# Kernel tuning notes

Measured on AMD Instinct MI355X. Metric: run time of the kernel, lower is better.

Reference implementation:

```python
import jax, jax.numpy as jnp
import numpy as np

B = 64        # num_groups
G = 32        # group_size
D = 2000      # output dim (counts per bin/gene)
M = 16        # m_samples
E = 16        # noise_dim
DIN = 256
LAM = 1.0
TRUST = 0.25
SMOOTH = 1e-8
IPF_ITERS = 60
EPS = 1e-12


def _arch(x, noise, W, b):
    # simple linear architecture: concat(x, noise) @ W + b
    return jnp.concatenate([x, noise], axis=-1) @ W + b


def _loss(x, target, W, b, noise_loss):
    # replicate each row m times (unsqueeze(1).expand(...).reshape == repeat)
    x_rep = jnp.repeat(x, M, axis=0)                      # [n*M, DIN]
    pred = _arch(x_rep, noise_loss, W, b)                 # [n*M, D] (no act_fn in loss path)
    pred = pred.reshape(B, G, M, D).sum(axis=1)           # [B, M, D]
    term_conf = jnp.linalg.norm(pred - target[:, None, :], axis=2).mean(axis=1)  # [B]
    sq = jnp.sum(pred * pred, axis=2)                     # [B, M]
    inn = jnp.einsum('bmd,bnd->bmn', pred, pred)          # [B, M, M]
    sqd = jnp.clip(sq[:, :, None] + sq[:, None, :] - 2.0 * inn, 1e-6)
    d = jnp.sqrt(sqd)
    mask = 1.0 - jnp.eye(M, dtype=d.dtype)
    mean_pd = jnp.sum(d * mask, axis=(1, 2)) / (M * (M - 1))
    return jnp.mean(term_conf - (LAM / 2.0) * mean_pd)


def _ipf(x_pred, C):
    # KL/I-projection with row anchoring (keep_rows=True, trust_clip=0.25)
    y = jnp.clip(x_pred, 0.0)
    C = jnp.clip(C.astype(y.dtype), 0.0)
    R = y.sum(axis=2)                                     # [B, G] anchor row totals
    col_zero = (y.sum(axis=1) <= 0) & (C > 0)
    y = y + SMOOTH * col_zero[:, None, :].astype(y.dtype)
    row_zero = (y.sum(axis=2) <= 0) & (R > 0)
    y = y + SMOOTH * row_zero[:, :, None].astype(y.dtype)

    def body(_, y):
        col = jnp.clip(y.sum(axis=1), EPS)
        y = y * jnp.clip(C / col, 1.0 - TRUST, 1.0 + TRUST)[:, None, :]
        row = jnp.clip(y.sum(axis=2), EPS)
        y = y * jnp.clip(R / row, 1.0 - TRUST, 1.0 + TRUST)[:, :, None]
        return y

    y = jax.lax.fori_loop(0, IPF_ITERS, body, y)
    col = jnp.clip(y.sum(axis=1), EPS)
    return y * (C / col)[:, None, :]


def _rank(v, descending):
    # rank along last axis via double argsort (0 = first picked)
    order = jnp.argsort(-v if descending else v, axis=-1)
    return jnp.argsort(order, axis=-1)


def _round_to_targets(x, target_bd):
    # exact integerization across G per (B, D); jit-safe full-G rank replaces dynamic-k topk+scatter
    x = jnp.clip(x, 0.0)
    xf = jnp.floor(x)
    y = xf.astype(jnp.int32)                              # [B, G, D]
    frac = x - xf
    need = target_bd - y.sum(axis=1)                      # [B, D]
    pos = jnp.clip(need, 0)
    q = pos // G
    y = y + q[:, None, :]
    r = pos - q * G
    rank = _rank(jnp.transpose(frac, (0, 2, 1)), descending=True)   # [B, D, G]
    add = (rank < r[:, :, None]).astype(jnp.int32)
    y = y + jnp.transpose(add, (0, 2, 1))
    # negative residuals: remove from smallest frac among y > 0
    need = target_bd - y.sum(axis=1)
    neg = jnp.clip(-need, 0)
    neg = jnp.minimum(neg, y.sum(axis=1))
    q = neg // G
    y_before = y
    y = jnp.clip(y - q[:, None, :], 0)
    removed = (y_before - y).sum(axis=1)
    r = neg - removed
    frac_m = jnp.where(y > 0, frac, jnp.inf)
    rank = _rank(jnp.transpose(frac_m, (0, 2, 1)), descending=False)
    rem = (rank < r[:, :, None]).astype(jnp.int32)
    y = jnp.clip(y - jnp.transpose(rem, (0, 2, 1)), 0)
    return y


def setup_inputs() -> dict:
    key = jax.random.key(0)
    ks = jax.random.split(key, 6)
    x = jax.random.normal(ks[0], (B * G, DIN), dtype=jnp.float32)
    target = jax.random.uniform(ks[1], (B, D), dtype=jnp.float32) * 100.0
    target_sum = jax.random.randint(ks[2], (B, D), 0, 200, dtype=jnp.int32)
    W = jax.random.normal(ks[3], (DIN + E, D), dtype=jnp.float32) * 0.02
    b = jnp.zeros((D,), dtype=jnp.float32)
    noise_loss = jax.random.normal(ks[4], (B * G * M, E), dtype=jnp.float32)
    noise_sample = jax.random.normal(ks[5], (B * G, E), dtype=jnp.float32)
    return {"x": x, "target": target, "target_sum": target_sum, "W": W, "b": b,
            "noise_loss": noise_loss, "noise_sample": noise_sample}


def reference(x, target, target_sum, W, b, noise_loss, noise_sample):
    loss = _loss(x, target, W, b, noise_loss)
    # conditional_sample pipeline (no-grad in original): softplus act (min_value==0)
    x_pred = jax.nn.softplus(_arch(x, noise_sample, W, b)).reshape(B, G, D)
    y_float = _ipf(x_pred, target_sum.astype(jnp.float32))
    y_int = _round_to_targets(y_float, target_sum.astype(jnp.int32))
    return loss, y_int.reshape(B * G, D)
```

## Files before the change

kernel.cpp:

```cpp
#include <hip/hip_runtime.h>
#include <math.h>

#define NB   64
#define NG   32
#define ND   2000
#define NM   16
#define NE   16
#define NDIN 256
#define NK   272

__device__ __forceinline__ float clampf(float v, float lo, float hi) {
    return fminf(fmaxf(v, lo), hi);
}

__device__ __forceinline__ float softplusf(float v) {
    return (v > 20.f) ? v : log1pf(expf(v));
}

__device__ __forceinline__ float readlane_f(float v, int lane) {
    return __int_as_float(__builtin_amdgcn_readlane(__float_as_int(v), lane));
}

__device__ __forceinline__ float wave_sum32(float v[NG], int lane) {
    {   const bool hi = (lane & 32) != 0;
        #pragma unroll
        for (int k = 0; k < 16; ++k) {
            float s = hi ? v[k] : v[k + 16];
            float r = __shfl_xor(s, 32);
            v[k] = (hi ? v[k + 16] : v[k]) + r;
        }
    }
    {   const bool hi = (lane & 16) != 0;
        #pragma unroll
        for (int k = 0; k < 8; ++k) {
            float s = hi ? v[k] : v[k + 8];
            float r = __shfl_xor(s, 16);
            v[k] = (hi ? v[k + 8] : v[k]) + r;
        }
    }
    {   const bool hi = (lane & 8) != 0;
        #pragma unroll
        for (int k = 0; k < 4; ++k) {
            float s = hi ? v[k] : v[k + 4];
            float r = __shfl_xor(s, 8);
            v[k] = (hi ? v[k + 4] : v[k]) + r;
        }
    }
    {   const bool hi = (lane & 4) != 0;
        #pragma unroll
        for (int k = 0; k < 2; ++k) {
            float s = hi ? v[k] : v[k + 2];
            float r = __shfl_xor(s, 4);
            v[k] = (hi ? v[k + 2] : v[k]) + r;
        }
    }
    {   const bool hi = (lane & 2) != 0;
        float s = hi ? v[0] : v[1];
        float r = __shfl_xor(s, 2);
        v[0] = (hi ? v[1] : v[0]) + r;
    }
    v[0] += __shfl_xor(v[0], 1);
    return v[0];
}

extern "C" __global__ __launch_bounds__(512)
void k_front(const float* __restrict__ x, const float* __restrict__ nl,
             const float* __restrict__ tgt, const float* __restrict__ W,
             const float* __restrict__ bias, const float* __restrict__ nsamp,
             float* __restrict__ xp, float* __restrict__ res2) {
    __shared__ __align__(16) float xr[NG * NK];
    __shared__ __align__(16) float ls[4800];
    const int q  = blockIdx.x;
    const int cx = q & 7, b = q >> 3;
    const int t  = threadIdx.x;

    for (int idx = t; idx < NG * NK; idx += 512) {
        const int g = idx / NK, c = idx - g * NK;
        const int row = b * NG + g;
        xr[idx] = (c < NDIN) ? x[(size_t)row * NDIN + c]
                             : nsamp[(size_t)row * NE + (c - NDIN)];
    }
    __syncthreads();

    if (t < 500) {
        const int d  = cx * 250 + (t >> 1);
        const int r0 = (t & 1) << 4;
        float acc[16];
        #pragma unroll
        for (int r = 0; r < 16; ++r) acc[r] = 0.f;
        for (int k = 0; k < NK; k += 4) {
            const float w0 = W[(size_t)(k + 0) * ND + d];
            const float w1 = W[(size_t)(k + 1) * ND + d];
            const float w2 = W[(size_t)(k + 2) * ND + d];
            const float w3 = W[(size_t)(k + 3) * ND + d];
            #pragma unroll
            for (int r = 0; r < 16; ++r) {
                const float4 xv = *(const float4*)&xr[(r0 + r) * NK + k];
                acc[r] += xv.x * w0 + xv.y * w1 + xv.z * w2 + xv.w * w3;
            }
        }
        const float bv = bias[d];
        #pragma unroll
        for (int r = 0; r < 16; ++r)
            xp[(size_t)(b * NG + r0 + r) * ND + d] = softplusf(acc[r] + bv);
    }

    if (t < 256) {
        float s = 0.f;
        for (int g = 0; g < NG; ++g) s += xr[g * NK + t];
        ls[t] = s;
        const float* nb = nl + (size_t)b * NG * (NM * NE);
        float s2 = 0.f;
        for (int g = 0; g < NG; ++g) s2 += nb[g * (NM * NE) + t];
        ls[256 + t] = s2;
    }

    int tm = 0, tn = 0;
    if (t >= 16 && t < 152) {
        int p = t - 16;
        for (int m = 0; m < NM; ++m) {
            int c = NM - m;
            if (p < c) { tm = m; tn = m + p; break; }
            p -= c;
        }
    }
    __syncthreads();

    float* xsl = ls;
    float* nsl = ls + 256;
    float* tgl = ls + 512;
    float* pt  = ls + 764;

    const int d = cx * 250 + t;
    if (t < 250) {
        tgl[t] = tgt[b * ND + d];
        float xw = 0.f;
        #pragma unroll 8
        for (int k = 0; k < NDIN; ++k) xw += xsl[k] * W[(size_t)k * ND + d];
        float we[NE];
        #pragma unroll
        for (int e = 0; e < NE; ++e) we[e] = W[(size_t)(NDIN + e) * ND + d];
        const float base0 = xw + (float)NG * bias[d];
        #pragma unroll
        for (int m = 0; m < NM; ++m) {
            float pm = base0;
            #pragma unroll
            for (int e = 0; e < NE; ++e) pm += nsl[m * NE + e] * we[e];
            pt[m * 252 + t] = pm;
        }
    }
    if (t < 32) {
        pt[(t >> 1) * 252 + 250 + (t & 1)] = 0.f;
        if (t < 2) tgl[250 + t] = 0.f;
    }
    __syncthreads();

    float acc = 0.f;
    if (t < 16) {
        const float4* pa  = (const float4*)&pt[t * 252];
        const float4* tga = (const float4*)&tgl[0];
        for (int i = 0; i < 63; ++i) {
            float4 pv = pa[i], tv = tga[i];
            float e0 = pv.x - tv.x, e1 = pv.y - tv.y, e2 = pv.z - tv.z, e3 = pv.w - tv.w;
            acc += e0 * e0 + e1 * e1 + e2 * e2 + e3 * e3;
        }
    } else if (t < 152) {
        const float4* pa = (const float4*)&pt[tm * 252];
        const float4* pb = (const float4*)&pt[tn * 252];
        for (int i = 0; i < 63; ++i) {
            float4 u = pa[i], v = pb[i];
            acc += u.x * v.x + u.y * v.y + u.z * v.z + u.w * v.w;
        }
    }
    if (t < 152) res2[((size_t)b * 8 + cx) * 152 + t] = acc;
}

__device__ __forceinline__ void ipf_path(
        const float* __restrict__ xp, const int* __restrict__ tsum,
        float* __restrict__ out, float* smem, int b, int t) {
    const int lane = t & 63, w = t >> 6;
    const int d0 = t * 4;
    const bool valid = (d0 < ND);
    const int g_own = (lane >> 1) & 31;

    float* wred = smem;

    float y0r[4][NG];
    #pragma unroll
    for (int g = 0; g < NG; ++g) {
        float4 v = make_float4(0.f, 0.f, 0.f, 0.f);
        if (valid) v = *(const float4*)(xp + (size_t)(b * NG + g) * ND + d0);
        y0r[0][g] = fmaxf(v.x, 0.f);
        y0r[1][g] = fmaxf(v.y, 0.f);
        y0r[2][g] = fmaxf(v.z, 0.f);
        y0r[3][g] = fmaxf(v.w, 0.f);
    }
    float Cc[4] = {0.f, 0.f, 0.f, 0.f};
    if (valid) {
        const int4 ci = *(const int4*)(tsum + (size_t)b * ND + d0);
        Cc[0] = (float)ci.x; Cc[1] = (float)ci.y; Cc[2] = (float)ci.z; Cc[3] = (float)ci.w;
    }
    float Ac[4] = {1.f, 1.f, 1.f, 1.f};
    float Bown = 1.f;
    float Rown;

    {
        float v[NG];
        #pragma unroll
        for (int g = 0; g < NG; ++g)
            v[g] = y0r[0][g] + y0r[1][g] + y0r[2][g] + y0r[3][g];
        const float tot = wave_sum32(v, lane);
        if ((lane & 1) == 0) wred[w * NG + g_own] = tot;
        __syncthreads();
        float s = 0.f;
        #pragma unroll
        for (int w2 = 0; w2 < 8; ++w2) s += wred[w2 * NG + g_own];
        Rown = s;
    }

    for (int q = 1; q <= 60; ++q) {
        float s0 = 0.f, s1 = 0.f, s2 = 0.f, s3 = 0.f;
        #pragma unroll
        for (int g = 0; g < NG; ++g) {
            const float bg = readlane_f(Bown, 2 * g);
            s0 += y0r[0][g] * bg; s1 += y0r[1][g] * bg;
            s2 += y0r[2][g] * bg; s3 += y0r[3][g] * bg;
        }
        Ac[0] *= clampf(Cc[0] / fmaxf(Ac[0] * s0, 1e-12f), 0.75f, 1.25f);
        Ac[1] *= clampf(Cc[1] / fmaxf(Ac[1] * s1, 1e-12f), 0.75f, 1.25f);
        Ac[2] *= clampf(Cc[2] / fmaxf(Ac[2] * s2, 1e-12f), 0.75f, 1.25f);
        Ac[3] *= clampf(Cc[3] / fmaxf(Ac[3] * s3, 1e-12f), 0.75f, 1.25f);
        float v[NG];
        #pragma unroll
        for (int g = 0; g < NG; ++g)
            v[g] = y0r[0][g] * Ac[0] + y0r[1][g] * Ac[1]
                 + y0r[2][g] * Ac[2] + y0r[3][g] * Ac[3];
        const float tot = wave_sum32(v, lane);
        const int buf = (q & 1) * (8 * NG);
        if ((lane & 1) == 0) wred[buf + w * NG + g_own] = tot;
        __syncthreads();
        float s = 0.f;
        #pragma unroll
        for (int w2 = 0; w2 < 8; ++w2) s += wred[buf + w2 * NG + g_own];
        Bown *= clampf(Rown / fmaxf(Bown * s, 1e-12f), 0.75f, 1.25f);
    }

    if (!valid) return;

    unsigned pk[NG];
    #pragma unroll
    for (int g = 0; g < NG; ++g) pk[g] = 0u;

    #pragma unroll
    for (int j = 0; j < 4; ++j) {
        float fr[NG];
        int   yv[NG];
        float s = 0.f;
        #pragma unroll
        for (int g = 0; g < NG; ++g) {
            const float z = y0r[j][g] * Ac[j] * readlane_f(Bown, 2 * g);
            fr[g] = z;
            s += z;
        }
        const float F = Cc[j] / fmaxf(s, 1e-12f);
        int isum = 0;
        #pragma unroll
        for (int g = 0; g < NG; ++g) {
            const float y = fr[g] * F;
            const float fl = floorf(y);
            yv[g] = (int)fl;
            fr[g] = y - fl;
            isum += yv[g];
        }
        const int Ci = (int)Cc[j];
        const int need = Ci - isum;
        const int pos = max(need, 0);
        const int q = pos >> 5;
        const int r = pos & 31;
        #pragma unroll
        for (int g = 0; g < NG; ++g) yv[g] += q;
        #pragma unroll
        for (int g = 0; g < NG; ++g) {
            int rank = 0;
            #pragma unroll
            for (int h = 0; h < NG; ++h) {
                if (h == g) continue;
                rank += (h < g) ? (fr[h] >= fr[g] ? 1 : 0) : (fr[h] > fr[g] ? 1 : 0);
            }
            if (rank < r) yv[g] += 1;
        }
        int neg = max(-need, 0);
        neg = min(neg, isum);
        if (__builtin_expect(neg > 0, 0)) {
            const int q2 = neg >> 5;
            int removed = 0;
            #pragma unroll
            for (int g = 0; g < NG; ++g) {
                const int yb = yv[g];
                const int yn = max(yb - q2, 0);
                removed += yb - yn;
                yv[g] = yn;
            }
            const int r2 = neg - removed;
            if (r2 > 0) {
                const float INF = __builtin_inff();
                #pragma unroll
                for (int g = 0; g < NG; ++g) {
                    const float fg = (yv[g] > 0) ? fr[g] : INF;
                    int rank = 0;
                    #pragma unroll
                    for (int h = 0; h < NG; ++h) {
                        if (h == g) continue;
                        const float fh = (yv[h] > 0) ? fr[h] : INF;
                        rank += (h < g) ? (fh <= fg ? 1 : 0) : (fh < fg ? 1 : 0);
                    }
                    if (rank < r2) yv[g] = max(yv[g] - 1, 0);
                }
            }
        }
        #pragma unroll
        for (int g = 0; g < NG; ++g)
            pk[g] |= ((unsigned)yv[g]) << (8 * j);
    }
    #pragma unroll
    for (int g = 0; g < NG; ++g) {
        float* op = &out[1 + (size_t)(b * NG + g) * ND + d0];
        op[0] = (float)(pk[g] & 0xffu);
        op[1] = (float)((pk[g] >> 8) & 0xffu);
        op[2] = (float)((pk[g] >> 16) & 0xffu);
        op[3] = (float)((pk[g] >> 24) & 0xffu);
    }
}

__device__ __forceinline__ void combine_path(
        const float* __restrict__ res2, float* __restrict__ out,
        float* ls, int t) {
    for (int idx = t; idx < NB * 152; idx += 512) {
        const int b = idx / 152, tau = idx - b * 152;
        float s = 0.f;
        #pragma unroll
        for (int c = 0; c < 8; ++c) s += res2[((size_t)b * 8 + c) * 152 + tau];
        ls[idx] = s;
    }
    __syncthreads();
    float v = 0.f;
    if (t < NB) {
        const float* res = &ls[t * 152];
        float conf = 0.f;
        for (int m = 0; m < NM; ++m) conf += sqrtf(res[m]);
        conf *= (1.f / NM);
        float pd = 0.f;
        for (int m = 0; m < NM; ++m) {
            const int offm = 16 + m * NM - m * (m - 1) / 2;
            const float sqm = res[offm];
            for (int n = m + 1; n < NM; ++n) {
                const int offn = 16 + n * NM - n * (n - 1) / 2;
                const float sqn = res[offn];
                const float inn = res[offm + (n - m)];
                pd += sqrtf(fmaxf(sqm + sqn - 2.f * inn, 1e-6f));
            }
        }
        pd = 2.f * pd / (float)(NM * (NM - 1));
        v = (conf - 0.5f * pd) * (1.f / NB);
    }
    if (t < 64) {
        #pragma unroll
        for (int o = 32; o >= 1; o >>= 1) v += __shfl_xor(v, o);
        if (t == 0) out[0] = v;
    }
}

extern "C" __global__ __launch_bounds__(512, 1)
void k_back(const float* __restrict__ xp, const int* __restrict__ tsum,
            const float* __restrict__ res2, float* __restrict__ out) {
    __shared__ float smem[NB * 152];
    const int bid = blockIdx.x;
    const int t = threadIdx.x;
    if (bid < NB) {
        ipf_path(xp, tsum, out, smem, bid, t);
    } else {
        combine_path(res2, out, smem, t);
    }
}

extern "C" void kernel_launch(void* const* d_in, const int* in_sizes, int n_in,
                              void* d_out, int out_size, void* d_ws, size_t ws_size,
                              hipStream_t stream) {
    const float* x     = (const float*)d_in[0];
    const float* tgt   = (const float*)d_in[1];
    const int*   tsum  = (const int*)d_in[2];
    const float* W     = (const float*)d_in[3];
    const float* bias  = (const float*)d_in[4];
    const float* nl    = (const float*)d_in[5];
    const float* nsamp = (const float*)d_in[6];
    float* out = (float*)d_out;

    (void)in_sizes; (void)n_in; (void)out_size; (void)ws_size;

    const size_t XPB = (size_t)2048 * 2000 * 4;
    float* xp   = (float*)d_ws;
    float* res2 = (float*)((char*)d_ws + XPB);

    hipLaunchKernelGGL(k_front, dim3(512), dim3(512), 0, stream,
                       x, nl, tgt, W, bias, nsamp, xp, res2);
    hipLaunchKernelGGL(k_back, dim3(NB + 1), dim3(512), 0, stream,
                       xp, tsum, res2, out);
}
```

Baseline: 337.8 us.

## Drop LDS staging in front GEMM and widen IPF to 8 columns per thread

The front kernel no longer stages x/noise rows in shared memory. Each wave now computes 8 rows by 2 adjacent columns, reading x directly from global memory (wave-uniform addresses) and W as float2. The IPF back kernel moves to 256 threads, each owning 8 columns, which halves the number of waves in the per-iteration cross-wave reduction and sync over 60 iterations. In exchange it doubles per-thread register state (256 y values), which risks spills, and the scalar global reads of x may cost more than the LDS path did.

```diff
diff --git a/kernel.cpp b/kernel.cpp
--- a/kernel.cpp
+++ b/kernel.cpp
@@ -68,51 +68,66 @@
              const float* __restrict__ tgt, const float* __restrict__ W,
              const float* __restrict__ bias, const float* __restrict__ nsamp,
              float* __restrict__ xp, float* __restrict__ res2) {
-    __shared__ __align__(16) float xr[NG * NK];
     __shared__ __align__(16) float ls[4800];
     const int q  = blockIdx.x;
     const int cx = q & 7, b = q >> 3;
     const int t  = threadIdx.x;
 
-    for (int idx = t; idx < NG * NK; idx += 512) {
-        const int g = idx / NK, c = idx - g * NK;
-        const int row = b * NG + g;
-        xr[idx] = (c < NDIN) ? x[(size_t)row * NDIN + c]
-                             : nsamp[(size_t)row * NE + (c - NDIN)];
-    }
-    __syncthreads();
-
-    if (t < 500) {
-        const int d  = cx * 250 + (t >> 1);
-        const int r0 = (t & 1) << 4;
-        float acc[16];
-        #pragma unroll
-        for (int r = 0; r < 16; ++r) acc[r] = 0.f;
-        for (int k = 0; k < NK; k += 4) {
-            const float w0 = W[(size_t)(k + 0) * ND + d];
-            const float w1 = W[(size_t)(k + 1) * ND + d];
-            const float w2 = W[(size_t)(k + 2) * ND + d];
-            const float w3 = W[(size_t)(k + 3) * ND + d];
-            #pragma unroll
-            for (int r = 0; r < 16; ++r) {
-                const float4 xv = *(const float4*)&xr[(r0 + r) * NK + k];
-                acc[r] += xv.x * w0 + xv.y * w1 + xv.z * w2 + xv.w * w3;
-            }
-        }
-        const float bv = bias[d];
-        #pragma unroll
-        for (int r = 0; r < 16; ++r)
-            xp[(size_t)(b * NG + r0 + r) * ND + d] = softplusf(acc[r] + bv);
-    }
+    {
+        const int wv   = __builtin_amdgcn_readfirstlane(t >> 6);
+        const int rh   = wv >> 1;
+        const int dh   = wv & 1;
+        const int lane = t & 63;
+        const int d    = cx * 256 + dh * 128 + 2 * lane;
+        if (d < ND) {
+            float acc[8][2];
+            #pragma unroll
+            for (int r = 0; r < 8; ++r) { acc[r][0] = 0.f; acc[r][1] = 0.f; }
+            const int row0 = b * NG + rh * 8;
+            for (int k = 0; k < NK; k += 4) {
+                const float2 w0 = *(const float2*)&W[(size_t)(k + 0) * ND + d];
+                const float2 w1 = *(const float2*)&W[(size_t)(k + 1) * ND + d];
+                const float2 w2 = *(const float2*)&W[(size_t)(k + 2) * ND + d];
+                const float2 w3 = *(const float2*)&W[(size_t)(k + 3) * ND + d];
+                #pragma unroll
+                for (int r = 0; r < 8; ++r) {
+                    float x0, x1, x2, x3;
+                    if (k < NDIN) {
+                        const float* xr = &x[(size_t)(row0 + r) * NDIN + k];
+                        x0 = xr[0]; x1 = xr[1]; x2 = xr[2]; x3 = xr[3];
+                    } else {
+                        const float* nr = &nsamp[(size_t)(row0 + r) * NE + (k - NDIN)];
+                        x0 = nr[0]; x1 = nr[1]; x2 = nr[2]; x3 = nr[3];
+                    }
+                    acc[r][0] += x0 * w0.x + x1 * w1.x + x2 * w2.x + x3 * w3.x;
+                    acc[r][1] += x0 * w0.y + x1 * w1.y + x2 * w2.y + x3 * w3.y;
+                }
+            }
+            const float2 bv = *(const float2*)&bias[d];
+            #pragma unroll
+            for (int r = 0; r < 8; ++r) {
+                float2 o;
+                o.x = softplusf(acc[r][0] + bv.x);
+                o.y = softplusf(acc[r][1] + bv.y);
+                *(float2*)&xp[(size_t)(row0 + r) * ND + d] = o;
+            }
+        }
+    }
+
+    float* xsl = ls;
+    float* nsl = ls + 256;
+    float* tgl = ls + 512;
+    float* pt  = ls + 764;
 
     if (t < 256) {
+        const float* xb = x + (size_t)b * NG * NDIN;
         float s = 0.f;
-        for (int g = 0; g < NG; ++g) s += xr[g * NK + t];
-        ls[t] = s;
+        for (int g = 0; g < NG; ++g) s += xb[g * NDIN + t];
+        xsl[t] = s;
         const float* nb = nl + (size_t)b * NG * (NM * NE);
         float s2 = 0.f;
         for (int g = 0; g < NG; ++g) s2 += nb[g * (NM * NE) + t];
-        ls[256 + t] = s2;
+        nsl[t] = s2;
     }
 
     int tm = 0, tn = 0;
@@ -125,11 +140,6 @@
         }
     }
     __syncthreads();
-
-    float* xsl = ls;
-    float* nsl = ls + 256;
-    float* tgl = ls + 512;
-    float* pt  = ls + 764;
 
     const int d = cx * 250 + t;
     if (t < 250) {
@@ -179,163 +189,180 @@
         const float* __restrict__ xp, const int* __restrict__ tsum,
         float* __restrict__ out, float* smem, int b, int t) {
     const int lane = t & 63, w = t >> 6;
-    const int d0 = t * 4;
+    const int d0 = t * 8;
     const bool valid = (d0 < ND);
     const int g_own = (lane >> 1) & 31;
 
     float* wred = smem;
 
-    float y0r[4][NG];
+    float y0r[8][NG];
     #pragma unroll
     for (int g = 0; g < NG; ++g) {
-        float4 v = make_float4(0.f, 0.f, 0.f, 0.f);
-        if (valid) v = *(const float4*)(xp + (size_t)(b * NG + g) * ND + d0);
-        y0r[0][g] = fmaxf(v.x, 0.f);
-        y0r[1][g] = fmaxf(v.y, 0.f);
-        y0r[2][g] = fmaxf(v.z, 0.f);
-        y0r[3][g] = fmaxf(v.w, 0.f);
-    }
-    float Cc[4] = {0.f, 0.f, 0.f, 0.f};
+        float4 v0 = make_float4(0.f, 0.f, 0.f, 0.f);
+        float4 v1 = make_float4(0.f, 0.f, 0.f, 0.f);
+        if (valid) {
+            const float* base = xp + (size_t)(b * NG + g) * ND + d0;
+            v0 = *(const float4*)(base);
+            v1 = *(const float4*)(base + 4);
+        }
+        y0r[0][g] = fmaxf(v0.x, 0.f); y0r[1][g] = fmaxf(v0.y, 0.f);
+        y0r[2][g] = fmaxf(v0.z, 0.f); y0r[3][g] = fmaxf(v0.w, 0.f);
+        y0r[4][g] = fmaxf(v1.x, 0.f); y0r[5][g] = fmaxf(v1.y, 0.f);
+        y0r[6][g] = fmaxf(v1.z, 0.f); y0r[7][g] = fmaxf(v1.w, 0.f);
+    }
+    float Cc[8];
+    #pragma unroll
+    for (int j = 0; j < 8; ++j) Cc[j] = 0.f;
     if (valid) {
-        const int4 ci = *(const int4*)(tsum + (size_t)b * ND + d0);
-        Cc[0] = (float)ci.x; Cc[1] = (float)ci.y; Cc[2] = (float)ci.z; Cc[3] = (float)ci.w;
-    }
-    float Ac[4] = {1.f, 1.f, 1.f, 1.f};
+        const int4 c0 = *(const int4*)(tsum + (size_t)b * ND + d0);
+        const int4 c1 = *(const int4*)(tsum + (size_t)b * ND + d0 + 4);
+        Cc[0] = (float)c0.x; Cc[1] = (float)c0.y; Cc[2] = (float)c0.z; Cc[3] = (float)c0.w;
+        Cc[4] = (float)c1.x; Cc[5] = (float)c1.y; Cc[6] = (float)c1.z; Cc[7] = (float)c1.w;
+    }
+    float Ac[8] = {1.f, 1.f, 1.f, 1.f, 1.f, 1.f, 1.f, 1.f};
     float Bown = 1.f;
     float Rown;
 
     {
         float v[NG];
         #pragma unroll
-        for (int g = 0; g < NG; ++g)
-            v[g] = y0r[0][g] + y0r[1][g] + y0r[2][g] + y0r[3][g];
+        for (int g = 0; g < NG; ++g) {
+            float s = y0r[0][g];
+            #pragma unroll
+            for (int j = 1; j < 8; ++j) s += y0r[j][g];
+            v[g] = s;
+        }
         const float tot = wave_sum32(v, lane);
         if ((lane & 1) == 0) wred[w * NG + g_own] = tot;
         __syncthreads();
-        float s = 0.f;
-        #pragma unroll
-        for (int w2 = 0; w2 < 8; ++w2) s += wred[w2 * NG + g_own];
-        Rown = s;
+        Rown = wred[0 * NG + g_own] + wred[1 * NG + g_own]
+             + wred[2 * NG + g_own] + wred[3 * NG + g_own];
     }
 
     for (int q = 1; q <= 60; ++q) {
-        float s0 = 0.f, s1 = 0.f, s2 = 0.f, s3 = 0.f;
+        float s[8];
+        #pragma unroll
+        for (int j = 0; j < 8; ++j) s[j] = 0.f;
         #pragma unroll
         for (int g = 0; g < NG; ++g) {
             const float bg = readlane_f(Bown, 2 * g);
-            s0 += y0r[0][g] * bg; s1 += y0r[1][g] * bg;
-            s2 += y0r[2][g] * bg; s3 += y0r[3][g] * bg;
-        }
-        Ac[0] *= clampf(Cc[0] / fmaxf(Ac[0] * s0, 1e-12f), 0.75f, 1.25f);
-        Ac[1] *= clampf(Cc[1] / fmaxf(Ac[1] * s1, 1e-12f), 0.75f, 1.25f);
-        Ac[2] *= clampf(Cc[2] / fmaxf(Ac[2] * s2, 1e-12f), 0.75f, 1.25f);
-        Ac[3] *= clampf(Cc[3] / fmaxf(Ac[3] * s3, 1e-12f), 0.75f, 1.25f);
+            #pragma unroll
+            for (int j = 0; j < 8; ++j) s[j] += y0r[j][g] * bg;
+        }
+        #pragma unroll
+        for (int j = 0; j < 8; ++j)
+            Ac[j] *= clampf(Cc[j] / fmaxf(Ac[j] * s[j], 1e-12f), 0.75f, 1.25f);
         float v[NG];
         #pragma unroll
-        for (int g = 0; g < NG; ++g)
-            v[g] = y0r[0][g] * Ac[0] + y0r[1][g] * Ac[1]
-                 + y0r[2][g] * Ac[2] + y0r[3][g] * Ac[3];
+        for (int g = 0; g < NG; ++g) {
+            float rv = y0r[0][g] * Ac[0];
+            #pragma unroll
+            for (int j = 1; j < 8; ++j) rv += y0r[j][g] * Ac[j];
+            v[g] = rv;
+        }
         const float tot = wave_sum32(v, lane);
-        const int buf = (q & 1) * (8 * NG);
+        const int buf = (q & 1) * (4 * NG);
         if ((lane & 1) == 0) wred[buf + w * NG + g_own] = tot;
         __syncthreads();
-        float s = 0.f;
-        #pragma unroll
-        for (int w2 = 0; w2 < 8; ++w2) s += wred[buf + w2 * NG + g_own];
-        Bown *= clampf(Rown / fmaxf(Bown * s, 1e-12f), 0.75f, 1.25f);
+        const float rs = wred[buf + 0 * NG + g_own] + wred[buf + 1 * NG + g_own]
+                       + wred[buf + 2 * NG + g_own] + wred[buf + 3 * NG + g_own];
+        Bown *= clampf(Rown / fmaxf(Bown * rs, 1e-12f), 0.75f, 1.25f);
     }
 
     if (!valid) return;
 
-    unsigned pk[NG];
     #pragma unroll
-    for (int g = 0; g < NG; ++g) pk[g] = 0u;
-
-    #pragma unroll
-    for (int j = 0; j < 4; ++j) {
-        float fr[NG];
-        int   yv[NG];
-        float s = 0.f;
-        #pragma unroll
-        for (int g = 0; g < NG; ++g) {
-            const float z = y0r[j][g] * Ac[j] * readlane_f(Bown, 2 * g);
-            fr[g] = z;
-            s += z;
-        }
-        const float F = Cc[j] / fmaxf(s, 1e-12f);
-        int isum = 0;
-        #pragma unroll
-        for (int g = 0; g < NG; ++g) {
-            const float y = fr[g] * F;
-            const float fl = floorf(y);
-            yv[g] = (int)fl;
-            fr[g] = y - fl;
-            isum += yv[g];
-        }
-        const int Ci = (int)Cc[j];
-        const int need = Ci - isum;
-        const int pos = max(need, 0);
-        const int q = pos >> 5;
-        const int r = pos & 31;
-        #pragma unroll
-        for (int g = 0; g < NG; ++g) yv[g] += q;
-        #pragma unroll
-        for (int g = 0; g < NG; ++g) {
-            int rank = 0;
-            #pragma unroll
-            for (int h = 0; h < NG; ++h) {
-                if (h == g) continue;
-                rank += (h < g) ? (fr[h] >= fr[g] ? 1 : 0) : (fr[h] > fr[g] ? 1 : 0);
-            }
-            if (rank < r) yv[g] += 1;
-        }
-        int neg = max(-need, 0);
-        neg = min(neg, isum);
-        if (__builtin_expect(neg > 0, 0)) {
-            const int q2 = neg >> 5;
-            int removed = 0;
+    for (int jh = 0; jh < 2; ++jh) {
+        unsigned pk[NG];
+        #pragma unroll
+        for (int g = 0; g < NG; ++g) pk[g] = 0u;
+        #pragma unroll
+        for (int jj = 0; jj < 4; ++jj) {
+            const int j = jh * 4 + jj;
+            float fr[NG];
+            int   yv[NG];
+            float s = 0.f;
             #pragma unroll
             for (int g = 0; g < NG; ++g) {
-                const int yb = yv[g];
-                const int yn = max(yb - q2, 0);
-                removed += yb - yn;
-                yv[g] = yn;
-            }
-            const int r2 = neg - removed;
-            if (r2 > 0) {
-                const float INF = __builtin_inff();
+                const float z = y0r[j][g] * Ac[j] * readlane_f(Bown, 2 * g);
+                fr[g] = z;
+                s += z;
+            }
+            const float F = Cc[j] / fmaxf(s, 1e-12f);
+            int isum = 0;
+            #pragma unroll
+            for (int g = 0; g < NG; ++g) {
+                const float y = fr[g] * F;
+                const float fl = floorf(y);
+                yv[g] = (int)fl;
+                fr[g] = y - fl;
+                isum += yv[g];
+            }
+            const int Ci = (int)Cc[j];
+            const int need = Ci - isum;
+            const int pos = max(need, 0);
+            const int q = pos >> 5;
+            const int r = pos & 31;
+            #pragma unroll
+            for (int g = 0; g < NG; ++g) yv[g] += q;
+            #pragma unroll
+            for (int g = 0; g < NG; ++g) {
+                int rank = 0;
+                #pragma unroll
+                for (int h = 0; h < NG; ++h) {
+                    if (h == g) continue;
+                    rank += (h < g) ? (fr[h] >= fr[g] ? 1 : 0) : (fr[h] > fr[g] ? 1 : 0);
+                }
+                if (rank < r) yv[g] += 1;
+            }
+            int neg = max(-need, 0);
+            neg = min(neg, isum);
+            if (__builtin_expect(neg > 0, 0)) {
+                const int q2 = neg >> 5;
+                int removed = 0;
                 #pragma unroll
                 for (int g = 0; g < NG; ++g) {
-                    const float fg = (yv[g] > 0) ? fr[g] : INF;
-                    int rank = 0;
+                    const int yb = yv[g];
+                    const int yn = max(yb - q2, 0);
+                    removed += yb - yn;
+                    yv[g] = yn;
+                }
+                const int r2 = neg - removed;
+                if (r2 > 0) {
+                    const float INF = __builtin_inff();
                     #pragma unroll
-                    for (int h = 0; h < NG; ++h) {
-                        if (h == g) continue;
-                        const float fh = (yv[h] > 0) ? fr[h] : INF;
-                        rank += (h < g) ? (fh <= fg ? 1 : 0) : (fh < fg ? 1 : 0);
+                    for (int g = 0; g < NG; ++g) {
+                        const float fg = (yv[g] > 0) ? fr[g] : INF;
+                        int rank = 0;
+                        #pragma unroll
+                        for (int h = 0; h < NG; ++h) {
+                            if (h == g) continue;
+                            const float fh = (yv[h] > 0) ? fr[h] : INF;
+                            rank += (h < g) ? (fh <= fg ? 1 : 0) : (fh < fg ? 1 : 0);
+                        }
+                        if (rank < r2) yv[g] = max(yv[g] - 1, 0);
                     }
-                    if (rank < r2) yv[g] = max(yv[g] - 1, 0);
                 }
             }
-        }
-        #pragma unroll
-        for (int g = 0; g < NG; ++g)
-            pk[g] |= ((unsigned)yv[g]) << (8 * j);
-    }
-    #pragma unroll
-    for (int g = 0; g < NG; ++g) {
-        float* op = &out[1 + (size_t)(b * NG + g) * ND + d0];
-        op[0] = (float)(pk[g] & 0xffu);
-        op[1] = (float)((pk[g] >> 8) & 0xffu);
-        op[2] = (float)((pk[g] >> 16) & 0xffu);
-        op[3] = (float)((pk[g] >> 24) & 0xffu);
+            #pragma unroll
+            for (int g = 0; g < NG; ++g)
+                pk[g] |= ((unsigned)yv[g]) << (8 * jj);
+        }
+        #pragma unroll
+        for (int g = 0; g < NG; ++g) {
+            float* op = &out[1 + (size_t)(b * NG + g) * ND + d0 + jh * 4];
+            op[0] = (float)(pk[g] & 0xffu);
+            op[1] = (float)((pk[g] >> 8) & 0xffu);
+            op[2] = (float)((pk[g] >> 16) & 0xffu);
+            op[3] = (float)((pk[g] >> 24) & 0xffu);
+        }
     }
 }
 
 __device__ __forceinline__ void combine_path(
         const float* __restrict__ res2, float* __restrict__ out,
         float* ls, int t) {
-    for (int idx = t; idx < NB * 152; idx += 512) {
+    for (int idx = t; idx < NB * 152; idx += 256) {
         const int b = idx / 152, tau = idx - b * 152;
         float s = 0.f;
         #pragma unroll
@@ -370,7 +397,7 @@
     }
 }
 
-extern "C" __global__ __launch_bounds__(512, 1)
+extern "C" __global__ __launch_bounds__(256, 1)
 void k_back(const float* __restrict__ xp, const int* __restrict__ tsum,
             const float* __restrict__ res2, float* __restrict__ out) {
     __shared__ float smem[NB * 152];
@@ -403,6 +430,6 @@
 
     hipLaunchKernelGGL(k_front, dim3(512), dim3(512), 0, stream,
                        x, nl, tgt, W, bias, nsamp, xp, res2);
-    hipLaunchKernelGGL(k_back, dim3(NB + 1), dim3(512), 0, stream,
+    hipLaunchKernelGGL(k_back, dim3(NB + 1), dim3(256), 0, stream,
                        xp, tsum, res2, out);
 }
```

Result: slower. 477.2 us (+41.3%).
